# Optimization experiments

Measured on AMD Instinct MI355X. Metric: run time of the kernel, lower is better.

## Reference

```python
import jax, jax.numpy as jnp
import numpy as np

B, N, C = 16, 2048, 384
CLUSTER_NUM = 512
K_NN = 5


def setup_inputs() -> dict:
    key = jax.random.key(0)
    k1, k2, k3, k4 = jax.random.split(key, 4)
    x = jax.random.normal(k1, (B, N, C), dtype=jnp.float32)
    idx_token = jax.random.randint(k2, (B, N), 0, N)
    agg_weight = jnp.ones((B, N, 1), dtype=jnp.float32)
    density_noise = jax.random.uniform(k3, (B, N), dtype=jnp.float32)
    score_w = jax.random.normal(k4, (1, C), dtype=jnp.float32) * 0.02
    score_b = jnp.zeros((1,), dtype=jnp.float32)
    return {"x": x, "idx_token": idx_token, "agg_weight": agg_weight,
            "density_noise": density_noise, "score_w": score_w, "score_b": score_b}


def _cluster_dpc_knn(x, density_noise, cluster_num, k):
    # x: [B,N,C]; clustering is done under no_grad in the original
    x = jax.lax.stop_gradient(x)
    b, n, c = x.shape
    sq = jnp.sum(x * x, axis=-1)  # [B,N]
    d2 = sq[:, :, None] + sq[:, None, :] - 2.0 * jnp.einsum('bnc,bmc->bnm', x, x)
    dist = jnp.sqrt(jnp.maximum(d2, 0.0)) / (c ** 0.5)  # [B,N,N] cdist/sqrt(C)
    # k smallest distances per row
    neg_near, _ = jax.lax.top_k(-dist, k)                # [B,N,k]
    density = jnp.exp(-jnp.mean(neg_near * neg_near, axis=-1))  # [B,N]
    density = density + density_noise * 1e-6             # tie-break noise
    mask = (density[:, None, :] > density[:, :, None]).astype(x.dtype)  # [B,N,N]
    dist_max = jnp.max(dist.reshape(b, -1), axis=-1)[:, None, None]
    dmin = jnp.min(dist * mask + dist_max * (1.0 - mask), axis=-1)  # [B,N]
    score = dmin * density
    _, index_down = jax.lax.top_k(score, cluster_num)    # [B,K] cluster centers
    dist_sub = jnp.take_along_axis(dist, index_down[:, :, None], axis=1)  # [B,K,N]
    idx_cluster = jnp.argmin(dist_sub, axis=1)           # [B,N]
    bi = jnp.arange(b)[:, None]
    centers = jnp.broadcast_to(jnp.arange(cluster_num)[None, :], (b, cluster_num))
    idx_cluster = idx_cluster.at[bi, index_down].set(centers)
    return idx_cluster, index_down


def reference(x, idx_token, agg_weight, density_noise, score_w, score_b):
    b, n, c = x.shape
    kc = CLUSTER_NUM
    # token score -> weight (equal_weight=False)
    token_weight = jnp.exp(x @ score_w.T + score_b)      # [B,N,1]
    idx_cluster, _ = _cluster_dpc_knn(x, density_noise, kc, K_NN)
    # merge tokens via segment sums
    bi = jnp.arange(b)[:, None]
    idx = (idx_cluster + bi * kc).reshape(-1)            # [B*N]
    all_weight = jax.ops.segment_sum(token_weight.reshape(-1, 1), idx,
                                     num_segments=b * kc) + 1e-6  # [B*K,1]
    norm_weight = token_weight / all_weight[idx].reshape(b, n, 1)
    x_merged = jax.ops.segment_sum((x * norm_weight).reshape(-1, c), idx,
                                   num_segments=b * kc).reshape(b, kc, c)
    idx_token_new = jnp.take_along_axis(idx_cluster, idx_token, axis=1)  # [B,N]
    weight_t = jnp.take_along_axis(norm_weight, idx_token[:, :, None], axis=1)
    agg_weight_new = agg_weight * weight_t               # [B,N,1]
    return x_merged, idx_token_new, agg_weight_new
```

## Files before the change

### kernel.cpp

```cpp
#include <hip/hip_runtime.h>
#include <math.h>

static constexpr int BB  = 16;
static constexpr int NN  = 2048;
static constexpr int CC  = 384;
static constexpr int KCL = 512;
static constexpr float RSQC = 0.051031036307982884f;

typedef short  bf16x8 __attribute__((ext_vector_type(8)));
typedef float  f32x4  __attribute__((ext_vector_type(4)));

__device__ __forceinline__ unsigned short f2b(float v) {
    unsigned u = __float_as_uint(v);
    unsigned r = (u + 0x7FFFu + ((u >> 16) & 1u)) >> 16;
    return (unsigned short)r;
}
__device__ __forceinline__ float b2f(unsigned short b) {
    return __uint_as_float(((unsigned)b) << 16);
}

__device__ __forceinline__ void gload16(const void* g, void* l) {
    __builtin_amdgcn_global_load_lds(
        (const __attribute__((address_space(1))) void*)g,
        (__attribute__((address_space(3))) void*)l, 16, 0, 0);
}

__global__ __launch_bounds__(256) void k_rowstats(
    const float* __restrict__ x, const float* __restrict__ sw,
    const float* __restrict__ sb, float* __restrict__ sq, float* __restrict__ tw)
{
    int row  = blockIdx.x * 4 + (threadIdx.x >> 6);
    int lane = threadIdx.x & 63;
    const float* xr = x + (size_t)row * CC;
    float s2 = 0.f, sd = 0.f;
    for (int c = lane; c < CC; c += 64) {
        float v = xr[c];
        s2 += v * v;
        sd += v * sw[c];
    }
    #pragma unroll
    for (int o = 32; o > 0; o >>= 1) {
        s2 += __shfl_down(s2, o);
        sd += __shfl_down(sd, o);
    }
    if (lane == 0) {
        sq[row] = s2;
        tw[row] = expf(sd + sb[0]);
    }
}

__global__ __launch_bounds__(256) void k_split(
    const float* __restrict__ x, unsigned short* __restrict__ Xh,
    unsigned short* __restrict__ Xl)
{
    size_t i = ((size_t)blockIdx.x * 256 + threadIdx.x) * 8;
    float4 v0 = *(const float4*)(x + i);
    float4 v1 = *(const float4*)(x + i + 4);
    float vv[8] = {v0.x, v0.y, v0.z, v0.w, v1.x, v1.y, v1.z, v1.w};
    unsigned short h[8], lo[8];
    #pragma unroll
    for (int e = 0; e < 8; ++e) {
        h[e]  = f2b(vv[e]);
        lo[e] = f2b(vv[e] - b2f(h[e]));
    }
    *(bf16x8*)(Xh + i) = *(bf16x8*)h;
    *(bf16x8*)(Xl + i) = *(bf16x8*)lo;
}


__global__ __launch_bounds__(256) void k_gemm_sym(
    const unsigned short* __restrict__ Xh, const unsigned short* __restrict__ Xl,
    const float* __restrict__ sq, float* __restrict__ D, int b0)
{
    const int b = b0 + blockIdx.z;
    int q = blockIdx.x;
    int ti = 0;
    while (q >= (16 - ti)) { q -= (16 - ti); ++ti; }
    const int tj = ti + q;
    const int i0 = ti * 128, j0 = tj * 128;

    const unsigned short* Xhb = Xh + (size_t)b * NN * CC;
    const unsigned short* Xlb = Xl + (size_t)b * NN * CC;
    const float* sqb = sq + b * NN;
    float* Db = D + (size_t)blockIdx.z * NN * NN;

    __shared__ union {
        unsigned short u16[4][128][32];
        float tr[64][129];
    } sm;

    const int t  = threadIdx.x;
    const int w  = t >> 6;
    const int l  = t & 63;
    const int wr = w >> 1, wc = w & 1;
    const int lt = l & 15, sl = l >> 4;

    f32x4 acc[4][4];
    #pragma unroll
    for (int fr = 0; fr < 4; ++fr)
        #pragma unroll
        for (int fc = 0; fc < 4; ++fc) acc[fr][fc] = (f32x4)0.0f;

    for (int kc = 0; kc < CC; kc += 32) {
        #pragma unroll
        for (int p = 0; p < 4; ++p) {
            const unsigned short* src = (p == 0) ? Xhb : (p == 1) ? Xlb
                                      : (p == 2) ? Xhb : Xlb;
            const int base0 = (p < 2) ? i0 : j0;
            #pragma unroll
            for (int u = 0; u < 2; ++u) {
                int seg = w * 2 + u;
                int r   = seg * 16 + (l >> 2);
                int s   = (l & 3) ^ (r & 3);
                const unsigned short* g = src + (size_t)(base0 + r) * CC + kc + s * 8;
                gload16(g, &sm.u16[p][seg * 16][0]);
            }
        }
        __syncthreads();

        bf16x8 fah[4], fal[4], fbh[4], fbl[4];
        #pragma unroll
        for (int fr = 0; fr < 4; ++fr) {
            int ra = wr * 64 + fr * 16 + lt;
            int sa = (sl ^ (ra & 3)) * 8;
            fah[fr] = *(const bf16x8*)&sm.u16[0][ra][sa];
            fal[fr] = *(const bf16x8*)&sm.u16[1][ra][sa];
        }
        #pragma unroll
        for (int fc = 0; fc < 4; ++fc) {
            int rb = wc * 64 + fc * 16 + lt;
            int sb_ = (sl ^ (rb & 3)) * 8;
            fbh[fc] = *(const bf16x8*)&sm.u16[2][rb][sb_];
            fbl[fc] = *(const bf16x8*)&sm.u16[3][rb][sb_];
        }
        #pragma unroll
        for (int fr = 0; fr < 4; ++fr)
            #pragma unroll
            for (int fc = 0; fc < 4; ++fc) {
                acc[fr][fc] = __builtin_amdgcn_mfma_f32_16x16x32_bf16(
                    fah[fr], fbh[fc], acc[fr][fc], 0, 0, 0);
                acc[fr][fc] = __builtin_amdgcn_mfma_f32_16x16x32_bf16(
                    fah[fr], fbl[fc], acc[fr][fc], 0, 0, 0);
                acc[fr][fc] = __builtin_amdgcn_mfma_f32_16x16x32_bf16(
                    fal[fr], fbh[fc], acc[fr][fc], 0, 0, 0);
            }
        __syncthreads();
    }

    float sqr[4][4], sqc[4];
    #pragma unroll
    for (int fr = 0; fr < 4; ++fr)
        #pragma unroll
        for (int reg = 0; reg < 4; ++reg)
            sqr[fr][reg] = sqb[i0 + wr * 64 + fr * 16 + sl * 4 + reg];
    #pragma unroll
    for (int fc = 0; fc < 4; ++fc)
        sqc[fc] = sqb[j0 + wc * 64 + fc * 16 + lt];

    #pragma unroll
    for (int fr = 0; fr < 4; ++fr)
        #pragma unroll
        for (int fc = 0; fc < 4; ++fc)
            #pragma unroll
            for (int reg = 0; reg < 4; ++reg) {
                int row = i0 + wr * 64 + fr * 16 + sl * 4 + reg;
                int col = j0 + wc * 64 + fc * 16 + lt;
                float d2 = fmaxf(sqr[fr][reg] + sqc[fc] - 2.0f * acc[fr][fc][reg], 0.0f);
                Db[(size_t)row * NN + col] = d2;
            }

    if (ti != tj) {
        #pragma unroll
        for (int h = 0; h < 2; ++h) {
            __syncthreads();
            if (wr == h) {
                #pragma unroll
                for (int fr = 0; fr < 4; ++fr)
                    #pragma unroll
                    for (int fc = 0; fc < 4; ++fc)
                        #pragma unroll
                        for (int reg = 0; reg < 4; ++reg) {
                            int rl = fr * 16 + sl * 4 + reg;
                            int cl = wc * 64 + fc * 16 + lt;
                            float d2 = fmaxf(sqr[fr][reg] + sqc[fc]
                                             - 2.0f * acc[fr][fc][reg], 0.0f);
                            sm.tr[rl][cl] = d2;
                        }
            }
            __syncthreads();
            for (int idx = t; idx < 128 * 64; idx += 256) {
                int c  = idx >> 6;
                int rl = idx & 63;
                Db[(size_t)(j0 + c) * NN + i0 + h * 64 + rl] = sm.tr[rl][c];
            }
        }
    }
}

__global__ __launch_bounds__(256) void k_density2(
    const float* __restrict__ D, const float* __restrict__ noise,
    float* __restrict__ dens, float* __restrict__ rowmax)
{
    int gid  = blockIdx.x * 4 + (threadIdx.x >> 6);
    int lane = threadIdx.x & 63;
    const float* row = D + (size_t)gid * NN;
    float t5[5] = {1e30f, 1e30f, 1e30f, 1e30f, 1e30f};
    float mx = 0.f;
    auto ins5 = [&](float v) {
        if (v < t5[4]) {
            t5[4] = v;
            #pragma unroll
            for (int q = 4; q > 0; --q) {
                if (t5[q] < t5[q - 1]) { float tmp = t5[q - 1]; t5[q - 1] = t5[q]; t5[q] = tmp; }
            }
        }
    };
    #pragma unroll
    for (int it = 0; it < 8; ++it) {
        float4 v = ((const float4*)row)[it * 64 + lane];
        mx = fmaxf(mx, fmaxf(fmaxf(v.x, v.y), fmaxf(v.z, v.w)));
        ins5(v.x); ins5(v.y); ins5(v.z); ins5(v.w);
    }
    #pragma unroll
    for (int o = 1; o < 64; o <<= 1) {
        float b0 = __shfl_xor(t5[0], o), b1 = __shfl_xor(t5[1], o);
        float b2 = __shfl_xor(t5[2], o), b3 = __shfl_xor(t5[3], o);
        float b4 = __shfl_xor(t5[4], o);
        mx = fmaxf(mx, __shfl_xor(mx, o));
        ins5(b0); ins5(b1); ins5(b2); ins5(b3); ins5(b4);
    }
    if (lane == 0) {
        float m2 = (t5[0] + t5[1] + t5[2] + t5[3] + t5[4]) * (1.0f / (5.0f * CC));
        dens[gid]   = expf(-m2) + noise[gid] * 1e-6f;
        rowmax[gid] = mx;
    }
}

__global__ __launch_bounds__(256) void k_distmax2(
    const float* __restrict__ rowmax, float* __restrict__ dmax)
{
    int b = blockIdx.x, t = threadIdx.x;
    float m = 0.f;
    for (int i = t; i < NN; i += 256) m = fmaxf(m, rowmax[b * NN + i]);
    __shared__ float red[256];
    red[t] = m; __syncthreads();
    for (int o = 128; o > 0; o >>= 1) {
        if (t < o) red[t] = fmaxf(red[t], red[t + o]);
        __syncthreads();
    }
    if (t == 0) dmax[b] = sqrtf(red[0]) * RSQC;
}

__global__ __launch_bounds__(256) void k_dmin2(
    const float* __restrict__ D, const float* __restrict__ dens,
    const float* __restrict__ dmax, float* __restrict__ score)
{
    int gid  = blockIdx.x * 4 + (threadIdx.x >> 6);
    int lane = threadIdx.x & 63;
    int bl   = gid >> 11;
    const float* row = D + (size_t)gid * NN;
    const float* dn  = dens + (size_t)bl * NN;
    float di = dens[gid];
    float m = 1e30f;
    #pragma unroll
    for (int it = 0; it < 8; ++it) {
        float4 v = ((const float4*)row)[it * 64 + lane];
        float4 dj = ((const float4*)dn)[it * 64 + lane];
        if (dj.x > di) m = fminf(m, v.x);
        if (dj.y > di) m = fminf(m, v.y);
        if (dj.z > di) m = fminf(m, v.z);
        if (dj.w > di) m = fminf(m, v.w);
    }
    #pragma unroll
    for (int o = 32; o > 0; o >>= 1) m = fminf(m, __shfl_down(m, o));
    if (lane == 0) {
        float dm = fminf(sqrtf(m) * RSQC, dmax[bl]);
        score[gid] = dm * di;
    }
}

__global__ __launch_bounds__(256) void k_assign2(
    const float* __restrict__ D, const int* __restrict__ idown,
    int* __restrict__ idxc)
{
    int bl = blockIdx.y;
    int tl = threadIdx.x & 63;
    int g  = threadIdx.x >> 6;
    int n  = blockIdx.x * 64 + tl;
    const float* Db = D + (size_t)bl * NN * NN;
    const int* idb  = idown + bl * KCL;
    float best = 1e30f; int bk = 0;
    for (int k = g * 128; k < (g + 1) * 128; ++k) {
        float v = Db[(size_t)idb[k] * NN + n];
        if (v < best) { best = v; bk = k; }
    }
    __shared__ float bvs[4][64];
    __shared__ int   bks[4][64];
    bvs[g][tl] = best; bks[g][tl] = bk;
    __syncthreads();
    if (threadIdx.x < 64) {
        float bv = bvs[0][threadIdx.x]; int bkk = bks[0][threadIdx.x];
        #pragma unroll
        for (int gg = 1; gg < 4; ++gg) {
            if (bvs[gg][threadIdx.x] < bv) { bv = bvs[gg][threadIdx.x]; bkk = bks[gg][threadIdx.x]; }
        }
        idxc[bl * NN + blockIdx.x * 64 + threadIdx.x] = bkk;
    }
}


__global__ __launch_bounds__(256) void k_density(
    const float* __restrict__ x, const float* __restrict__ sq,
    const float* __restrict__ noise, float* __restrict__ dens,
    float* __restrict__ rowmax)
{
    const int b  = blockIdx.y;
    const int i0 = blockIdx.x * 64;
    const float* xb  = x + (size_t)b * NN * CC;
    const float* sqb = sq + b * NN;
    __shared__ float As[16][64];
    __shared__ float Bs[16][64];
    __shared__ float mrg[64][16][5];
    __shared__ float mrgmax[64][16];
    const int t  = threadIdx.x;
    const int tx = t & 15, ty = t >> 4;
    const int lr = t >> 2, lk4 = (t & 3) * 4;

    float top[4][5];
    float rmax[4];
    float sqi[4];
    #pragma unroll
    for (int r = 0; r < 4; ++r) {
        sqi[r]  = sqb[i0 + ty * 4 + r];
        rmax[r] = 0.f;
        #pragma unroll
        for (int q = 0; q < 5; ++q) top[r][q] = 1e30f;
    }

    for (int j0 = 0; j0 < NN; j0 += 64) {
        float acc[4][4];
        #pragma unroll
        for (int r = 0; r < 4; ++r)
            #pragma unroll
            for (int s = 0; s < 4; ++s) acc[r][s] = 0.f;

        for (int k0 = 0; k0 < CC; k0 += 16) {
            float4 av = *(const float4*)(xb + (size_t)(i0 + lr) * CC + k0 + lk4);
            float4 bv = *(const float4*)(xb + (size_t)(j0 + lr) * CC + k0 + lk4);
            As[lk4 + 0][lr] = av.x; As[lk4 + 1][lr] = av.y;
            As[lk4 + 2][lr] = av.z; As[lk4 + 3][lr] = av.w;
            Bs[lk4 + 0][lr] = bv.x; Bs[lk4 + 1][lr] = bv.y;
            Bs[lk4 + 2][lr] = bv.z; Bs[lk4 + 3][lr] = bv.w;
            __syncthreads();
            #pragma unroll
            for (int kk = 0; kk < 16; ++kk) {
                float4 a4 = *(const float4*)&As[kk][ty * 4];
                float4 b4 = *(const float4*)&Bs[kk][tx * 4];
                float ar[4] = {a4.x, a4.y, a4.z, a4.w};
                float br[4] = {b4.x, b4.y, b4.z, b4.w};
                #pragma unroll
                for (int r = 0; r < 4; ++r)
                    #pragma unroll
                    for (int s = 0; s < 4; ++s)
                        acc[r][s] = fmaf(ar[r], br[s], acc[r][s]);
            }
            __syncthreads();
        }
        float sqj[4];
        #pragma unroll
        for (int s = 0; s < 4; ++s) sqj[s] = sqb[j0 + tx * 4 + s];
        #pragma unroll
        for (int r = 0; r < 4; ++r) {
            #pragma unroll
            for (int s = 0; s < 4; ++s) {
                float d2 = sqi[r] + sqj[s] - 2.0f * acc[r][s];
                float d  = sqrtf(fmaxf(d2, 0.0f)) * RSQC;
                rmax[r] = fmaxf(rmax[r], d);
                if (d < top[r][4]) {
                    top[r][4] = d;
                    #pragma unroll
                    for (int q = 4; q > 0; --q) {
                        if (top[r][q] < top[r][q - 1]) {
                            float tmp = top[r][q - 1];
                            top[r][q - 1] = top[r][q];
                            top[r][q] = tmp;
                        }
                    }
                }
            }
        }
    }
    #pragma unroll
    for (int r = 0; r < 4; ++r) {
        #pragma unroll
        for (int q = 0; q < 5; ++q) mrg[ty * 4 + r][tx][q] = top[r][q];
        mrgmax[ty * 4 + r][tx] = rmax[r];
    }
    __syncthreads();
    if (t < 64) {
        float t5[5] = {1e30f, 1e30f, 1e30f, 1e30f, 1e30f};
        float mx = 0.f;
        for (int c = 0; c < 16; ++c) {
            mx = fmaxf(mx, mrgmax[t][c]);
            #pragma unroll
            for (int q = 0; q < 5; ++q) {
                float d = mrg[t][c][q];
                if (d < t5[4]) {
                    t5[4] = d;
                    #pragma unroll
                    for (int u = 4; u > 0; --u) {
                        if (t5[u] < t5[u - 1]) {
                            float tmp = t5[u - 1]; t5[u - 1] = t5[u]; t5[u] = tmp;
                        }
                    }
                }
            }
        }
        float m2 = (t5[0]*t5[0] + t5[1]*t5[1] + t5[2]*t5[2] +
                    t5[3]*t5[3] + t5[4]*t5[4]) / 5.0f;
        int i = i0 + t;
        dens[b * NN + i]   = expf(-m2) + noise[b * NN + i] * 1e-6f;
        rowmax[b * NN + i] = mx;
    }
}

__global__ __launch_bounds__(256) void k_distmax(
    const float* __restrict__ rowmax, float* __restrict__ dmax)
{
    int b = blockIdx.x, t = threadIdx.x;
    float m = 0.f;
    for (int i = t; i < NN; i += 256) m = fmaxf(m, rowmax[b * NN + i]);
    __shared__ float red[256];
    red[t] = m; __syncthreads();
    for (int o = 128; o > 0; o >>= 1) {
        if (t < o) red[t] = fmaxf(red[t], red[t + o]);
        __syncthreads();
    }
    if (t == 0) dmax[b] = red[0];
}

__global__ __launch_bounds__(256) void k_dmin(
    const float* __restrict__ x, const float* __restrict__ sq,
    const float* __restrict__ dens, const float* __restrict__ dmax,
    float* __restrict__ score)
{
    const int b  = blockIdx.y;
    const int i0 = blockIdx.x * 64;
    const float* xb  = x + (size_t)b * NN * CC;
    const float* sqb = sq + b * NN;
    const float* dnb = dens + b * NN;
    __shared__ float As[16][64];
    __shared__ float Bs[16][64];
    __shared__ float mrgmin[64][16];
    const int t  = threadIdx.x;
    const int tx = t & 15, ty = t >> 4;
    const int lr = t >> 2, lk4 = (t & 3) * 4;

    float sqi[4], di[4], mn[4];
    #pragma unroll
    for (int r = 0; r < 4; ++r) {
        sqi[r] = sqb[i0 + ty * 4 + r];
        di[r]  = dnb[i0 + ty * 4 + r];
        mn[r]  = 1e30f;
    }

    for (int j0 = 0; j0 < NN; j0 += 64) {
        float acc[4][4];
        #pragma unroll
        for (int r = 0; r < 4; ++r)
            #pragma unroll
            for (int s = 0; s < 4; ++s) acc[r][s] = 0.f;

        for (int k0 = 0; k0 < CC; k0 += 16) {
            float4 av = *(const float4*)(xb + (size_t)(i0 + lr) * CC + k0 + lk4);
            float4 bv = *(const float4*)(xb + (size_t)(j0 + lr) * CC + k0 + lk4);
            As[lk4 + 0][lr] = av.x; As[lk4 + 1][lr] = av.y;
            As[lk4 + 2][lr] = av.z; As[lk4 + 3][lr] = av.w;
            Bs[lk4 + 0][lr] = bv.x; Bs[lk4 + 1][lr] = bv.y;
            Bs[lk4 + 2][lr] = bv.z; Bs[lk4 + 3][lr] = bv.w;
            __syncthreads();
            #pragma unroll
            for (int kk = 0; kk < 16; ++kk) {
                float4 a4 = *(const float4*)&As[kk][ty * 4];
                float4 b4 = *(const float4*)&Bs[kk][tx * 4];
                float ar[4] = {a4.x, a4.y, a4.z, a4.w};
                float br[4] = {b4.x, b4.y, b4.z, b4.w};
                #pragma unroll
                for (int r = 0; r < 4; ++r)
                    #pragma unroll
                    for (int s = 0; s < 4; ++s)
                        acc[r][s] = fmaf(ar[r], br[s], acc[r][s]);
            }
            __syncthreads();
        }
        float dj[4];
        #pragma unroll
        for (int s = 0; s < 4; ++s) dj[s] = dnb[j0 + tx * 4 + s];
        float sqj[4];
        #pragma unroll
        for (int s = 0; s < 4; ++s) sqj[s] = sqb[j0 + tx * 4 + s];
        #pragma unroll
        for (int r = 0; r < 4; ++r) {
            #pragma unroll
            for (int s = 0; s < 4; ++s) {
                float d2 = sqi[r] + sqj[s] - 2.0f * acc[r][s];
                float d  = sqrtf(fmaxf(d2, 0.0f)) * RSQC;
                if (dj[s] > di[r]) mn[r] = fminf(mn[r], d);
            }
        }
    }
    #pragma unroll
    for (int r = 0; r < 4; ++r) mrgmin[ty * 4 + r][tx] = mn[r];
    __syncthreads();
    if (t < 64) {
        float m = 1e30f;
        for (int c = 0; c < 16; ++c) m = fminf(m, mrgmin[t][c]);
        float dm = fminf(dmax[b], m);
        score[b * NN + i0 + t] = dm * dnb[i0 + t];
    }
}

__global__ __launch_bounds__(256) void k_assign(
    const float* __restrict__ x, const float* __restrict__ sq,
    const int* __restrict__ idown, int* __restrict__ idxc)
{
    const int b  = blockIdx.y;
    const int n0 = blockIdx.x * 64;
    const float* xb  = x + (size_t)b * NN * CC;
    const float* sqb = sq + b * NN;
    const int* idb = idown + b * KCL;
    __shared__ float As[16][64];
    __shared__ float Bs[16][64];
    __shared__ float mv[64][16];
    __shared__ int   mk[64][16];
    const int t  = threadIdx.x;
    const int tx = t & 15, ty = t >> 4;
    const int lr = t >> 2, lk4 = (t & 3) * 4;

    float sqt[4];
    #pragma unroll
    for (int s = 0; s < 4; ++s) sqt[s] = sqb[n0 + tx * 4 + s];
    float bestv[4] = {1e30f, 1e30f, 1e30f, 1e30f};
    int   bestk[4] = {0, 0, 0, 0};

    for (int c0 = 0; c0 < KCL; c0 += 64) {
        int crow = idb[c0 + lr];
        float acc[4][4];
        #pragma unroll
        for (int r = 0; r < 4; ++r)
            #pragma unroll
            for (int s = 0; s < 4; ++s) acc[r][s] = 0.f;

        for (int k0 = 0; k0 < CC; k0 += 16) {
            float4 av = *(const float4*)(xb + (size_t)crow * CC + k0 + lk4);
            float4 bv = *(const float4*)(xb + (size_t)(n0 + lr) * CC + k0 + lk4);
            As[lk4 + 0][lr] = av.x; As[lk4 + 1][lr] = av.y;
            As[lk4 + 2][lr] = av.z; As[lk4 + 3][lr] = av.w;
            Bs[lk4 + 0][lr] = bv.x; Bs[lk4 + 1][lr] = bv.y;
            Bs[lk4 + 2][lr] = bv.z; Bs[lk4 + 3][lr] = bv.w;
            __syncthreads();
            #pragma unroll
            for (int kk = 0; kk < 16; ++kk) {
                float4 a4 = *(const float4*)&As[kk][ty * 4];
                float4 b4 = *(const float4*)&Bs[kk][tx * 4];
                float ar[4] = {a4.x, a4.y, a4.z, a4.w};
                float br[4] = {b4.x, b4.y, b4.z, b4.w};
                #pragma unroll
                for (int r = 0; r < 4; ++r)
                    #pragma unroll
                    for (int s = 0; s < 4; ++s)
                        acc[r][s] = fmaf(ar[r], br[s], acc[r][s]);
            }
            __syncthreads();
        }
        float sqc[4];
        #pragma unroll
        for (int r = 0; r < 4; ++r) sqc[r] = sqb[idb[c0 + ty * 4 + r]];
        #pragma unroll
        for (int r = 0; r < 4; ++r) {
            int kg = c0 + ty * 4 + r;
            #pragma unroll
            for (int s = 0; s < 4; ++s) {
                float e = fmaxf(sqc[r] + sqt[s] - 2.0f * acc[r][s], 0.0f);
                if (e < bestv[s]) { bestv[s] = e; bestk[s] = kg; }
            }
        }
    }
    #pragma unroll
    for (int s = 0; s < 4; ++s) {
        mv[tx * 4 + s][ty] = bestv[s];
        mk[tx * 4 + s][ty] = bestk[s];
    }
    __syncthreads();
    if (t < 64) {
        float bv = 1e30f; int bk = 1 << 30;
        for (int c = 0; c < 16; ++c) {
            float v = mv[t][c]; int k = mk[t][c];
            if (v < bv || (v == bv && k < bk)) { bv = v; bk = k; }
        }
        idxc[b * NN + n0 + t] = bk;
    }
}


__global__ __launch_bounds__(1024) void k_topk(
    const float* __restrict__ score, int* __restrict__ idown)
{
    int b = blockIdx.x, t = threadIdx.x;
    __shared__ float s[NN];
    __shared__ int   si[NN];
    s[t]         = score[b * NN + t];        si[t]        = t;
    s[t + 1024]  = score[b * NN + t + 1024]; si[t + 1024] = t + 1024;
    __syncthreads();
    for (int k = 2; k <= NN; k <<= 1) {
        for (int j = k >> 1; j > 0; j >>= 1) {
            int i = (t & (j - 1)) | ((t & ~(j - 1)) << 1);
            int l = i | j;
            bool dir = ((i & k) == 0);
            float svi = s[i], svl = s[l];
            int   ii  = si[i], il = si[l];
            bool before_l_i = (svl > svi) || (svl == svi && il < ii);
            if (before_l_i == dir) {
                s[i] = svl; s[l] = svi;
                si[i] = il; si[l] = ii;
            }
            __syncthreads();
        }
    }
    if (t < KCL) idown[b * KCL + t] = si[t];
}

__global__ __launch_bounds__(256) void k_override(
    const int* __restrict__ idown, int* __restrict__ idxc)
{
    int g = blockIdx.x * 256 + threadIdx.x;
    int b = g >> 9, k = g & 511;
    idxc[b * NN + idown[g]] = k;
}

__global__ __launch_bounds__(512) void k_merge(
    const float* __restrict__ x, const float* __restrict__ tw,
    const int* __restrict__ idxc, float* __restrict__ aw, float* __restrict__ xm)
{
    int b = blockIdx.y, k = blockIdx.x;
    __shared__ int members[NN];
    __shared__ int wc[8];
    __shared__ float red[512];
    int t = threadIdx.x, lane = t & 63, w = t >> 6;
    const int* ib = idxc + b * NN;
    int base = 0;
    for (int r0 = 0; r0 < NN; r0 += 512) {
        int n = r0 + t;
        bool m = (ib[n] == k);
        unsigned long long msk = __ballot(m);
        if (lane == 0) wc[w] = __popcll(msk);
        __syncthreads();
        int off = 0;
        for (int ww = 0; ww < w; ++ww) off += wc[ww];
        int tot = 0;
        #pragma unroll
        for (int ww = 0; ww < 8; ++ww) tot += wc[ww];
        if (m) members[base + off + __popcll(msk & ((1ull << lane) - 1ull))] = n;
        base += tot;
        __syncthreads();
    }
    int cnt = base;
    const float* twb = tw + b * NN;
    float ps = 0.f;
    for (int p = t; p < cnt; p += 512) ps += twb[members[p]];
    red[t] = ps; __syncthreads();
    for (int o = 256; o > 0; o >>= 1) {
        if (t < o) red[t] += red[t + o];
        __syncthreads();
    }
    float awf = red[0] + 1e-6f;
    if (t == 0) aw[b * KCL + k] = awf;
    if (t < CC) {
        const float* xb = x + (size_t)b * NN * CC;
        float s = 0.f;
        for (int p = 0; p < cnt; ++p) {
            int n = members[p];
            s += xb[(size_t)n * CC + t] * twb[n];
        }
        xm[((size_t)b * KCL + k) * CC + t] = s / awf;
    }
}

__global__ __launch_bounds__(256) void k_out(
    const int* __restrict__ idx_token, const float* __restrict__ aggw,
    const float* __restrict__ tw, const float* __restrict__ aw,
    const int* __restrict__ idxc, float* __restrict__ out_idx,
    float* __restrict__ out_agg)
{
    int g = blockIdx.x * 256 + threadIdx.x;
    int b = g >> 11;
    int it = idx_token[g];
    int kclu = idxc[b * NN + it];
    out_idx[g] = (float)kclu;
    float nw = tw[b * NN + it] / aw[b * KCL + kclu];
    out_agg[g] = aggw[g] * nw;
}

extern "C" void kernel_launch(void* const* d_in, const int* in_sizes, int n_in,
                              void* d_out, int out_size, void* d_ws, size_t ws_size,
                              hipStream_t stream) {
    const float* x         = (const float*)d_in[0];
    const int*   idx_token = (const int*)  d_in[1];
    const float* aggw      = (const float*)d_in[2];
    const float* noise     = (const float*)d_in[3];
    const float* sw        = (const float*)d_in[4];
    const float* sb        = (const float*)d_in[5];

    float* ws      = (float*)d_ws;
    float* sq      = ws;
    float* tw      = ws + 32768;
    float* dens    = ws + 65536;
    float* rowmax  = ws + 98304;
    float* score   = ws + 131072;
    float* dmax    = ws + 163840;
    float* aw      = ws + 163904;
    int*   idown   = (int*)(ws + 172096);
    int*   idxc    = (int*)(ws + 180288);

    unsigned short* Xh = (unsigned short*)(ws + 213056);
    unsigned short* Xl = (unsigned short*)(ws + 213056 + 6291456);
    float* Dbuf        = ws + 213056 + 2 * 6291456;

    const size_t head_bytes = (size_t)(213056 + 2 * 6291456) * 4;
    size_t avail = (ws_size > head_bytes) ? (ws_size - head_bytes) : 0;
    int nbg = 0;
    for (int g = 16; g >= 1; g >>= 1) {
        if ((size_t)g * NN * NN * 4 <= avail) { nbg = g; break; }
    }

    float* xm      = (float*)d_out;
    float* out_idx = xm + (size_t)BB * KCL * CC;
    float* out_agg = out_idx + (size_t)BB * NN;

    k_rowstats<<<dim3(BB * NN / 4), 256, 0, stream>>>(x, sw, sb, sq, tw);

    if (nbg >= 1) {
        k_split<<<dim3(BB * NN * CC / (256 * 8)), 256, 0, stream>>>(x, Xh, Xl);
        for (int b0 = 0; b0 < BB; b0 += nbg) {
            k_gemm_sym<<<dim3(136, 1, nbg), 256, 0, stream>>>(Xh, Xl, sq, Dbuf, b0);
            k_density2<<<dim3(nbg * NN / 4), 256, 0, stream>>>(Dbuf, noise + b0 * NN,
                                                              dens + b0 * NN, rowmax + b0 * NN);
            k_distmax2<<<dim3(nbg), 256, 0, stream>>>(rowmax + b0 * NN, dmax + b0);
            k_dmin2   <<<dim3(nbg * NN / 4), 256, 0, stream>>>(Dbuf, dens + b0 * NN,
                                                              dmax + b0, score + b0 * NN);
            k_topk    <<<dim3(nbg), 1024, 0, stream>>>(score + b0 * NN, idown + b0 * KCL);
            k_assign2 <<<dim3(NN / 64, nbg), 256, 0, stream>>>(Dbuf, idown + b0 * KCL,
                                                               idxc + b0 * NN);
            k_override<<<dim3(nbg * KCL / 256), 256, 0, stream>>>(idown + b0 * KCL,
                                                                  idxc + b0 * NN);
        }
    } else {
        k_density <<<dim3(NN / 64, BB), 256, 0, stream>>>(x, sq, noise, dens, rowmax);
        k_distmax <<<dim3(BB), 256, 0, stream>>>(rowmax, dmax);
        k_dmin    <<<dim3(NN / 64, BB), 256, 0, stream>>>(x, sq, dens, dmax, score);
        k_topk    <<<dim3(BB), 1024, 0, stream>>>(score, idown);
        k_assign  <<<dim3(NN / 64, BB), 256, 0, stream>>>(x, sq, idown, idxc);
        k_override<<<dim3(BB * KCL / 256), 256, 0, stream>>>(idown, idxc);
    }

    k_merge<<<dim3(KCL, BB), 512, 0, stream>>>(x, tw, idxc, aw, xm);
    k_out  <<<dim3(BB * NN / 256), 256, 0, stream>>>(idx_token, aggw, tw, aw, idxc,
                                                     out_idx, out_agg);
}
```

Before: 456.0 us.

## Double-buffer GEMM LDS tiles and batch pipeline in groups of four

The symmetric distance GEMM now double-buffers its LDS tiles, so the next K-chunk's global-to-LDS loads are issued while the MFMAs run on the current chunk. The XOR swizzle also changes to use (r>>1)&3, aiming to cut LDS bank conflicts. When the workspace can hold all 16 distance matrices, the per-batch kernels run in groups of 4, and topk, assign and override each launch once over all batches, giving fewer and larger launches. In exchange, LDS use per block doubles, which may lower occupancy.

Measured after the change: 455.0 us. No clear change (-0.2%).

```diff
diff --git a/kernel.cpp b/kernel.cpp
--- a/kernel.cpp
+++ b/kernel.cpp
@@ -85,7 +85,7 @@
     float* Db = D + (size_t)blockIdx.z * NN * NN;
 
     __shared__ union {
-        unsigned short u16[4][128][32];
+        unsigned short u16[2][4][128][32];
         float tr[64][129];
     } sm;
 
@@ -101,7 +101,7 @@
         #pragma unroll
         for (int fc = 0; fc < 4; ++fc) acc[fr][fc] = (f32x4)0.0f;
 
-    for (int kc = 0; kc < CC; kc += 32) {
+    auto STAGE = [&](int bi, int kc) {
         #pragma unroll
         for (int p = 0; p < 4; ++p) {
             const unsigned short* src = (p == 0) ? Xhb : (p == 1) ? Xlb
@@ -111,27 +111,33 @@
             for (int u = 0; u < 2; ++u) {
                 int seg = w * 2 + u;
                 int r   = seg * 16 + (l >> 2);
-                int s   = (l & 3) ^ (r & 3);
-                const unsigned short* g = src + (size_t)(base0 + r) * CC + kc + s * 8;
-                gload16(g, &sm.u16[p][seg * 16][0]);
-            }
-        }
-        __syncthreads();
+                int s   = (l & 3) ^ ((r >> 1) & 3);
+                gload16(src + (size_t)(base0 + r) * CC + kc + s * 8,
+                        &sm.u16[bi][p][seg * 16][0]);
+            }
+        }
+    };
+
+    STAGE(0, 0);
+    __syncthreads();
+    int cur = 0;
+    for (int ch = 0; ch < CC / 32; ++ch) {
+        if (ch + 1 < CC / 32) STAGE(cur ^ 1, (ch + 1) * 32);
 
         bf16x8 fah[4], fal[4], fbh[4], fbl[4];
         #pragma unroll
         for (int fr = 0; fr < 4; ++fr) {
             int ra = wr * 64 + fr * 16 + lt;
-            int sa = (sl ^ (ra & 3)) * 8;
-            fah[fr] = *(const bf16x8*)&sm.u16[0][ra][sa];
-            fal[fr] = *(const bf16x8*)&sm.u16[1][ra][sa];
+            int sa = (sl ^ ((ra >> 1) & 3)) * 8;
+            fah[fr] = *(const bf16x8*)&sm.u16[cur][0][ra][sa];
+            fal[fr] = *(const bf16x8*)&sm.u16[cur][1][ra][sa];
         }
         #pragma unroll
         for (int fc = 0; fc < 4; ++fc) {
             int rb = wc * 64 + fc * 16 + lt;
-            int sb_ = (sl ^ (rb & 3)) * 8;
-            fbh[fc] = *(const bf16x8*)&sm.u16[2][rb][sb_];
-            fbl[fc] = *(const bf16x8*)&sm.u16[3][rb][sb_];
+            int sb_ = (sl ^ ((rb >> 1) & 3)) * 8;
+            fbh[fc] = *(const bf16x8*)&sm.u16[cur][2][rb][sb_];
+            fbl[fc] = *(const bf16x8*)&sm.u16[cur][3][rb][sb_];
         }
         #pragma unroll
         for (int fr = 0; fr < 4; ++fr)
@@ -145,6 +151,7 @@
                     fal[fr], fbh[fc], acc[fr][fc], 0, 0, 0);
             }
         __syncthreads();
+        cur ^= 1;
     }
 
     float sqr[4][4], sqc[4];
@@ -739,7 +746,22 @@
 
     k_rowstats<<<dim3(BB * NN / 4), 256, 0, stream>>>(x, sw, sb, sq, tw);
 
-    if (nbg >= 1) {
+    if (nbg >= 16) {
+        k_split<<<dim3(BB * NN * CC / (256 * 8)), 256, 0, stream>>>(x, Xh, Xl);
+        const int G = 4;
+        for (int b0 = 0; b0 < BB; b0 += G) {
+            float* Dg = Dbuf + (size_t)b0 * NN * NN;
+            k_gemm_sym<<<dim3(136, 1, G), 256, 0, stream>>>(Xh, Xl, sq, Dg, b0);
+            k_density2<<<dim3(G * NN / 4), 256, 0, stream>>>(Dg, noise + b0 * NN,
+                                                             dens + b0 * NN, rowmax + b0 * NN);
+            k_distmax2<<<dim3(G), 256, 0, stream>>>(rowmax + b0 * NN, dmax + b0);
+            k_dmin2   <<<dim3(G * NN / 4), 256, 0, stream>>>(Dg, dens + b0 * NN,
+                                                             dmax + b0, score + b0 * NN);
+        }
+        k_topk    <<<dim3(BB), 1024, 0, stream>>>(score, idown);
+        k_assign2 <<<dim3(NN / 64, BB), 256, 0, stream>>>(Dbuf, idown, idxc);
+        k_override<<<dim3(BB * KCL / 256), 256, 0, stream>>>(idown, idxc);
+    } else if (nbg >= 1) {
         k_split<<<dim3(BB * NN * CC / (256 * 8)), 256, 0, stream>>>(x, Xh, Xl);
         for (int b0 = 0; b0 < BB; b0 += nbg) {
             k_gemm_sym<<<dim3(136, 1, nbg), 256, 0, stream>>>(Xh, Xl, sq, Dbuf, b0);
```
